# Performance work log

Measured on AMD Instinct MI355X. Metric: run time of the kernel, lower is better.

Reference implementation:

```python
import jax, jax.numpy as jnp
import numpy as np

EPSILON = 1.0
SIGMA = 1.0
CUTOFF = 5.0
SHIFT = 4.0 * EPSILON * ((SIGMA / CUTOFF) ** 12 - (SIGMA / CUTOFF) ** 6)

N_ATOMS = 100000
N_EDGES = 6400000


def setup_inputs() -> dict:
    key = jax.random.key(0)
    k1, k2, k3 = jax.random.split(key, 3)
    distances = jax.random.normal(k1, (N_EDGES, 3), dtype=jnp.float32)
    first_atom = jax.random.randint(k2, (N_EDGES,), 0, N_ATOMS, dtype=jnp.int64)
    second_atom = jax.random.randint(k3, (N_EDGES,), 0, N_ATOMS, dtype=jnp.int64)
    return {
        "distances": distances,
        "first_atom": first_atom,
        "second_atom": second_atom,
        "n_atoms": N_ATOMS,
    }


def reference(distances, first_atom, second_atom, n_atoms):
    # per-edge LJ energy: r = |d|, e = 4*eps*((sigma/r)^12 - (sigma/r)^6) - shift
    r = jnp.linalg.norm(distances, axis=1)  # [E]
    sr6 = (SIGMA / r) ** 6
    sr12 = sr6 * sr6
    e = 4.0 * EPSILON * (sr12 - sr6) - SHIFT  # [E]
    # half-list: each edge contributes e/2 to both endpoints
    half_e = 0.5 * e
    energy = jax.ops.segment_sum(half_e, first_atom, num_segments=n_atoms)
    energy = energy + jax.ops.segment_sum(half_e, second_atom, num_segments=n_atoms)
    return energy  # [n_atoms] per-atom energies
```

## Files before the change

kernel.cpp:

```cpp
#include <hip/hip_runtime.h>

__device__ __constant__ float kShift = 4.0f * (float)(1.0 / 244140625.0 - 1.0 / 15625.0);

#define GROUPS 3
#define MAX_MEMBERS 85
#define BUCKET 33334
#define BLOCK_T 1024

__device__ __forceinline__ float lj_half_e(float x, float y, float z) {
    float r2 = x * x + y * y + z * z;
    float inv_r2 = 1.0f / r2;
    float sr6 = inv_r2 * inv_r2 * inv_r2;
    float sr12 = sr6 * sr6;
    float e = 4.0f * (sr12 - sr6) - kShift;
    return 0.5f * e;
}

__global__ __launch_bounds__(BLOCK_T) void lj_gather_group(
        const float* __restrict__ dist,
        const int* __restrict__ atom_a,
        const int* __restrict__ atom_b,
        float* __restrict__ ws,
        int members, int n_edges) {
    __shared__ float acc[BUCKET];

    const int g = blockIdx.x / members;
    const int m = blockIdx.x % members;
    const unsigned lo = (unsigned)(g * BUCKET);

    for (int i = threadIdx.x; i < BUCKET; i += BLOCK_T) acc[i] = 0.0f;
    __syncthreads();

    const long long quads = ((long long)n_edges + 3) / 4;
    const long long per = (quads + members - 1) / members;
    const long long q0 = (long long)m * per;
    const long long q1 = (q0 + per < quads) ? (q0 + per) : quads;

    for (long long q = q0 + threadIdx.x; q < q1; q += BLOCK_T) {
        long long e0 = q * 4;
        if (e0 + 3 < n_edges) {
            const float4* d4 = (const float4*)(dist) + (size_t)q * 3;
            float4 v0 = d4[0];
            float4 v1 = d4[1];
            float4 v2 = d4[2];
            int4 ia = ((const int4*)atom_a)[q];
            int4 ib = ((const int4*)atom_b)[q];

            float h0 = lj_half_e(v0.x, v0.y, v0.z);
            float h1 = lj_half_e(v0.w, v1.x, v1.y);
            float h2 = lj_half_e(v1.z, v1.w, v2.x);
            float h3 = lj_half_e(v2.y, v2.z, v2.w);

            unsigned r;
            r = (unsigned)ia.x - lo; if (r < BUCKET) atomicAdd(&acc[r], h0);
            r = (unsigned)ib.x - lo; if (r < BUCKET) atomicAdd(&acc[r], h0);
            r = (unsigned)ia.y - lo; if (r < BUCKET) atomicAdd(&acc[r], h1);
            r = (unsigned)ib.y - lo; if (r < BUCKET) atomicAdd(&acc[r], h1);
            r = (unsigned)ia.z - lo; if (r < BUCKET) atomicAdd(&acc[r], h2);
            r = (unsigned)ib.z - lo; if (r < BUCKET) atomicAdd(&acc[r], h2);
            r = (unsigned)ia.w - lo; if (r < BUCKET) atomicAdd(&acc[r], h3);
            r = (unsigned)ib.w - lo; if (r < BUCKET) atomicAdd(&acc[r], h3);
        } else {
            for (long long e = e0; e < n_edges; ++e) {
                float x = dist[e * 3 + 0];
                float y = dist[e * 3 + 1];
                float z = dist[e * 3 + 2];
                float h = lj_half_e(x, y, z);
                unsigned r;
                r = (unsigned)atom_a[e] - lo; if (r < BUCKET) atomicAdd(&acc[r], h);
                r = (unsigned)atom_b[e] - lo; if (r < BUCKET) atomicAdd(&acc[r], h);
            }
        }
    }
    __syncthreads();

    float* dst = ws + (size_t)blockIdx.x * BUCKET;
    for (int i = threadIdx.x; i < BUCKET; i += BLOCK_T) dst[i] = acc[i];
}

__global__ void reduce_groups(const float* __restrict__ ws,
                              float* __restrict__ out,
                              int members, int n_atoms) {
    int i = blockIdx.x * blockDim.x + threadIdx.x;
    if (i >= n_atoms) return;
    int g = i / BUCKET;
    int off = i - g * BUCKET;
    const float* base = ws + ((size_t)g * members) * BUCKET + off;
    float s = 0.0f;
    for (int b = 0; b < members; ++b) s += base[(size_t)b * BUCKET];
    out[i] = s;
}

__global__ void lj_scatter_direct(const float* __restrict__ dist,
                                  const int* __restrict__ atom_a,
                                  const int* __restrict__ atom_b,
                                  float* __restrict__ out,
                                  int n_edges) {
    int t = blockIdx.x * blockDim.x + threadIdx.x;
    long long e0 = (long long)t * 4;
    if (e0 >= n_edges) return;
    if (e0 + 3 < n_edges) {
        const float4* d4 = (const float4*)(dist) + (size_t)t * 3;
        float4 v0 = d4[0];
        float4 v1 = d4[1];
        float4 v2 = d4[2];
        int4 ia = ((const int4*)atom_a)[t];
        int4 ib = ((const int4*)atom_b)[t];
        float h0 = lj_half_e(v0.x, v0.y, v0.z);
        float h1 = lj_half_e(v0.w, v1.x, v1.y);
        float h2 = lj_half_e(v1.z, v1.w, v2.x);
        float h3 = lj_half_e(v2.y, v2.z, v2.w);
        atomicAdd(&out[ia.x], h0);
        atomicAdd(&out[ib.x], h0);
        atomicAdd(&out[ia.y], h1);
        atomicAdd(&out[ib.y], h1);
        atomicAdd(&out[ia.z], h2);
        atomicAdd(&out[ib.z], h2);
        atomicAdd(&out[ia.w], h3);
        atomicAdd(&out[ib.w], h3);
    } else {
        for (long long e = e0; e < n_edges; ++e) {
            float x = dist[e * 3 + 0];
            float y = dist[e * 3 + 1];
            float z = dist[e * 3 + 2];
            float h = lj_half_e(x, y, z);
            atomicAdd(&out[atom_a[e]], h);
            atomicAdd(&out[atom_b[e]], h);
        }
    }
}

extern "C" void kernel_launch(void* const* d_in, const int* in_sizes, int n_in,
                              void* d_out, int out_size, void* d_ws, size_t ws_size,
                              hipStream_t stream) {
    const float* dist = (const float*)d_in[0];
    const int* atom_a = (const int*)d_in[1];
    const int* atom_b = (const int*)d_in[2];
    float* out = (float*)d_out;

    int n_edges = in_sizes[1];
    int n_atoms = out_size;

    size_t per_member = (size_t)GROUPS * BUCKET * sizeof(float);
    int members = (int)(ws_size / per_member);
    if (members > MAX_MEMBERS) members = MAX_MEMBERS;
    bool range_ok = ((long long)GROUPS * BUCKET >= (long long)n_atoms);

    if (members >= 8 && range_ok) {
        float* ws = (float*)d_ws;
        lj_gather_group<<<GROUPS * members, BLOCK_T, 0, stream>>>(
            dist, atom_a, atom_b, ws, members, n_edges);
        int rblock = 256;
        int rgrid = (n_atoms + rblock - 1) / rblock;
        reduce_groups<<<rgrid, rblock, 0, stream>>>(ws, out, members, n_atoms);
    } else {
        hipMemsetAsync(d_out, 0, (size_t)n_atoms * sizeof(float), stream);
        int n_quads = (n_edges + 3) / 4;
        int block = 256;
        int grid = (n_quads + block - 1) / block;
        lj_scatter_direct<<<grid, block, 0, stream>>>(dist, atom_a, atom_b, out, n_edges);
    }
}
```

Before: 211.3 us.

## Route a fraction of each edge chunk through global atomics to cut redundant group scans

Every group previously scanned every edge and kept only hits in its own LDS bucket, so the edge stream was read three times. Now the first ninth of each member's chunk is processed by a single group, which scatters directly into a zeroed global accumulator with global atomics. The other groups skip that part, and the reduce kernel adds the global accumulator to its sum. This trades some redundant reads and compute for slower global atomics, an extra memset and load imbalance, since the blocks that take the global slice do more work.

```diff
diff --git a/kernel.cpp b/kernel.cpp
--- a/kernel.cpp
+++ b/kernel.cpp
@@ -3,9 +3,11 @@
 __device__ __constant__ float kShift = 4.0f * (float)(1.0 / 244140625.0 - 1.0 / 15625.0);
 
 #define GROUPS 3
-#define MAX_MEMBERS 85
+#define MAX_MEMBERS 84
 #define BUCKET 33334
 #define BLOCK_T 1024
+#define GFRAC 9
+
 
 __device__ __forceinline__ float lj_half_e(float x, float y, float z) {
     float r2 = x * x + y * y + z * z;
@@ -16,11 +18,12 @@
     return 0.5f * e;
 }
 
-__global__ __launch_bounds__(BLOCK_T) void lj_gather_group(
+__global__ __launch_bounds__(BLOCK_T) void lj_gather_hybrid(
         const float* __restrict__ dist,
         const int* __restrict__ atom_a,
         const int* __restrict__ atom_b,
         float* __restrict__ ws,
+        float* __restrict__ gacc,
         int members, int n_edges) {
     __shared__ float acc[BUCKET];
 
@@ -31,54 +34,79 @@
     for (int i = threadIdx.x; i < BUCKET; i += BLOCK_T) acc[i] = 0.0f;
     __syncthreads();
 
-    const long long quads = ((long long)n_edges + 3) / 4;
+    const long long quads = (long long)n_edges >> 2;
     const long long per = (quads + members - 1) / members;
     const long long q0 = (long long)m * per;
-    const long long q1 = (q0 + per < quads) ? (q0 + per) : quads;
+    const long long qe = (q0 + per < quads) ? (q0 + per) : quads;
+    const long long span = (qe > q0) ? (qe - q0) : 0;
+    const long long gq = span / GFRAC;
 
-    for (long long q = q0 + threadIdx.x; q < q1; q += BLOCK_T) {
-        long long e0 = q * 4;
-        if (e0 + 3 < n_edges) {
+    if ((m % GROUPS) == g) {
+        for (long long q = q0 + threadIdx.x; q < q0 + gq; q += BLOCK_T) {
             const float4* d4 = (const float4*)(dist) + (size_t)q * 3;
             float4 v0 = d4[0];
             float4 v1 = d4[1];
             float4 v2 = d4[2];
             int4 ia = ((const int4*)atom_a)[q];
             int4 ib = ((const int4*)atom_b)[q];
-
             float h0 = lj_half_e(v0.x, v0.y, v0.z);
             float h1 = lj_half_e(v0.w, v1.x, v1.y);
             float h2 = lj_half_e(v1.z, v1.w, v2.x);
             float h3 = lj_half_e(v2.y, v2.z, v2.w);
+            atomicAdd(&gacc[ia.x], h0);
+            atomicAdd(&gacc[ib.x], h0);
+            atomicAdd(&gacc[ia.y], h1);
+            atomicAdd(&gacc[ib.y], h1);
+            atomicAdd(&gacc[ia.z], h2);
+            atomicAdd(&gacc[ib.z], h2);
+            atomicAdd(&gacc[ia.w], h3);
+            atomicAdd(&gacc[ib.w], h3);
+        }
+    }
 
-            unsigned r;
-            r = (unsigned)ia.x - lo; if (r < BUCKET) atomicAdd(&acc[r], h0);
-            r = (unsigned)ib.x - lo; if (r < BUCKET) atomicAdd(&acc[r], h0);
-            r = (unsigned)ia.y - lo; if (r < BUCKET) atomicAdd(&acc[r], h1);
-            r = (unsigned)ib.y - lo; if (r < BUCKET) atomicAdd(&acc[r], h1);
-            r = (unsigned)ia.z - lo; if (r < BUCKET) atomicAdd(&acc[r], h2);
-            r = (unsigned)ib.z - lo; if (r < BUCKET) atomicAdd(&acc[r], h2);
-            r = (unsigned)ia.w - lo; if (r < BUCKET) atomicAdd(&acc[r], h3);
-            r = (unsigned)ib.w - lo; if (r < BUCKET) atomicAdd(&acc[r], h3);
-        } else {
-            for (long long e = e0; e < n_edges; ++e) {
-                float x = dist[e * 3 + 0];
-                float y = dist[e * 3 + 1];
-                float z = dist[e * 3 + 2];
-                float h = lj_half_e(x, y, z);
-                unsigned r;
-                r = (unsigned)atom_a[e] - lo; if (r < BUCKET) atomicAdd(&acc[r], h);
-                r = (unsigned)atom_b[e] - lo; if (r < BUCKET) atomicAdd(&acc[r], h);
-            }
+    for (long long q = q0 + gq + threadIdx.x; q < qe; q += BLOCK_T) {
+        const float4* d4 = (const float4*)(dist) + (size_t)q * 3;
+        float4 v0 = d4[0];
+        float4 v1 = d4[1];
+        float4 v2 = d4[2];
+        int4 ia = ((const int4*)atom_a)[q];
+        int4 ib = ((const int4*)atom_b)[q];
+
+        float h0 = lj_half_e(v0.x, v0.y, v0.z);
+        float h1 = lj_half_e(v0.w, v1.x, v1.y);
+        float h2 = lj_half_e(v1.z, v1.w, v2.x);
+        float h3 = lj_half_e(v2.y, v2.z, v2.w);
+
+        unsigned u;
+        u = (unsigned)ia.x - lo; if (u < BUCKET) atomicAdd(&acc[u], h0);
+        u = (unsigned)ib.x - lo; if (u < BUCKET) atomicAdd(&acc[u], h0);
+        u = (unsigned)ia.y - lo; if (u < BUCKET) atomicAdd(&acc[u], h1);
+        u = (unsigned)ib.y - lo; if (u < BUCKET) atomicAdd(&acc[u], h1);
+        u = (unsigned)ia.z - lo; if (u < BUCKET) atomicAdd(&acc[u], h2);
+        u = (unsigned)ib.z - lo; if (u < BUCKET) atomicAdd(&acc[u], h2);
+        u = (unsigned)ia.w - lo; if (u < BUCKET) atomicAdd(&acc[u], h3);
+        u = (unsigned)ib.w - lo; if (u < BUCKET) atomicAdd(&acc[u], h3);
+    }
+
+    if ((n_edges & 3) && m == members - 1) {
+        for (long long e = quads * 4 + threadIdx.x; e < n_edges; e += BLOCK_T) {
+            float x = dist[e * 3 + 0];
+            float y = dist[e * 3 + 1];
+            float z = dist[e * 3 + 2];
+            float h = lj_half_e(x, y, z);
+            unsigned u;
+            u = (unsigned)atom_a[e] - lo; if (u < BUCKET) atomicAdd(&acc[u], h);
+            u = (unsigned)atom_b[e] - lo; if (u < BUCKET) atomicAdd(&acc[u], h);
         }
     }
     __syncthreads();
 
-    float* dst = ws + (size_t)blockIdx.x * BUCKET;
+    float* dst = ws + (size_t)(g * members + m) * BUCKET;
     for (int i = threadIdx.x; i < BUCKET; i += BLOCK_T) dst[i] = acc[i];
 }
 
 __global__ void reduce_groups(const float* __restrict__ ws,
+                              const float* __restrict__ gacc,
                               float* __restrict__ out,
                               int members, int n_atoms) {
     int i = blockIdx.x * blockDim.x + threadIdx.x;
@@ -86,7 +114,8 @@
     int g = i / BUCKET;
     int off = i - g * BUCKET;
     const float* base = ws + ((size_t)g * members) * BUCKET + off;
-    float s = 0.0f;
+    float s = gacc[i];
+    #pragma unroll 4
     for (int b = 0; b < members; ++b) s += base[(size_t)b * BUCKET];
     out[i] = s;
 }
@@ -141,18 +170,22 @@
     int n_edges = in_sizes[1];
     int n_atoms = out_size;
 
+    size_t gacc_bytes = (size_t)n_atoms * sizeof(float);
     size_t per_member = (size_t)GROUPS * BUCKET * sizeof(float);
-    int members = (int)(ws_size / per_member);
+    size_t avail = (ws_size > gacc_bytes) ? (ws_size - gacc_bytes) : 0;
+    int members = (int)(avail / per_member);
     if (members > MAX_MEMBERS) members = MAX_MEMBERS;
     bool range_ok = ((long long)GROUPS * BUCKET >= (long long)n_atoms);
 
     if (members >= 8 && range_ok) {
         float* ws = (float*)d_ws;
-        lj_gather_group<<<GROUPS * members, BLOCK_T, 0, stream>>>(
-            dist, atom_a, atom_b, ws, members, n_edges);
+        float* gacc = ws + (size_t)GROUPS * members * BUCKET;
+        hipMemsetAsync(gacc, 0, gacc_bytes, stream);
+        lj_gather_hybrid<<<GROUPS * members, BLOCK_T, 0, stream>>>(
+            dist, atom_a, atom_b, ws, gacc, members, n_edges);
         int rblock = 256;
         int rgrid = (n_atoms + rblock - 1) / rblock;
-        reduce_groups<<<rgrid, rblock, 0, stream>>>(ws, out, members, n_atoms);
+        reduce_groups<<<rgrid, rblock, 0, stream>>>(ws, gacc, out, members, n_atoms);
     } else {
         hipMemsetAsync(d_out, 0, (size_t)n_atoms * sizeof(float), stream);
         int n_quads = (n_edges + 3) / 4;
```

Result: slower. 240.2 us (+13.7%).
